# Performance work log

Measured on AMD Instinct MI355X. Metric: run time of the kernel, lower is better.

The kernel has to match this reference:

```python
import jax, jax.numpy as jnp
import numpy as np

WIN = 400   # args.win_size
K = 8       # args.topk_k


def setup_inputs() -> dict:
    key = jax.random.key(0)
    k1, k2, k3 = jax.random.split(key, 3)
    mixed = jax.random.normal(k1, (2, 400000), dtype=jnp.float32)       # [bs, n_snps]
    ref = jax.random.normal(k2, (3, 64, 400000), dtype=jnp.float32)     # [n_anc, n_refs, n_snps]
    weights = jax.random.uniform(k3, (K, 1), dtype=jnp.float32)         # AddPoolings.weights
    return {"mixed": mixed, "ref": ref, "weights": weights}


def reference(mixed, ref, weights):
    # fast_windowed_distances: broadcast multiply then windowed mean
    # mixed: [B, S], ref: [A, R, S] -> prod: [B, A, R, S]
    prod = mixed[:, None, None, :] * ref[None, :, :, :]
    B, A, R, S = prod.shape
    n_windows = S // WIN
    win_mean = prod.reshape(B, A, R, n_windows, WIN).mean(axis=-1)  # [B, A, R, W]
    # TopKPool.shared_refpanel: topk over the reference dim (R)
    scores = jnp.transpose(win_mean, (0, 1, 3, 2))       # [B, A, W, R]
    vals, idx = jax.lax.top_k(scores, K)                 # [B, A, W, K]
    # AddPoolings.shared_refpanel: weighted sum over the k dim
    out = jnp.sum(vals * weights[:K, 0], axis=-1)        # [B, A, W]
    return out, idx
```

## Files before the change

### kernel.cpp

```cpp
#include <hip/hip_runtime.h>
#include <math.h>

#define WIN   400
#define NREF  64
#define KTOP  8
#define NSNP  400000
#define NB    2
#define NA    3
#define NW    1000

__global__ __launch_bounds__(256, 4) void topk_window_kernel(
    const float* __restrict__ mixed,
    const float* __restrict__ ref,
    const float* __restrict__ weights,
    float* __restrict__ out)
{
    __shared__ float smix[NB][WIN];
    __shared__ float winvals[NB][NREF];

    const int bid  = blockIdx.x;
    const int a    = bid / NW;
    const int w    = bid % NW;
    const int tid  = threadIdx.x;
    const int lane = tid & 63;
    const int wave = tid >> 6;

    if (tid < NB * (WIN / 4)) {
        const int b  = tid / (WIN / 4);
        const int j4 = tid % (WIN / 4);
        const float4 v =
            reinterpret_cast<const float4*>(mixed + (size_t)b * NSNP + (size_t)w * WIN)[j4];
        reinterpret_cast<float4*>(&smix[b][0])[j4] = v;
    }
    __syncthreads();

    const float4* m0p = reinterpret_cast<const float4*>(&smix[0][0]);
    const float4* m1p = reinterpret_cast<const float4*>(&smix[1][0]);
    for (int r = wave; r < NREF; r += 4) {
        const float4* row = reinterpret_cast<const float4*>(
            ref + (size_t)(a * NREF + r) * NSNP + (size_t)w * WIN);
        float4 rv = row[lane];
        float4 m0 = m0p[lane];
        float4 m1 = m1p[lane];
        float acc0 = rv.x * m0.x + rv.y * m0.y + rv.z * m0.z + rv.w * m0.w;
        float acc1 = rv.x * m1.x + rv.y * m1.y + rv.z * m1.z + rv.w * m1.w;
        if (lane < (WIN / 4) - 64) {
            float4 rv2 = row[lane + 64];
            float4 n0  = m0p[lane + 64];
            float4 n1  = m1p[lane + 64];
            acc0 += rv2.x * n0.x + rv2.y * n0.y + rv2.z * n0.z + rv2.w * n0.w;
            acc1 += rv2.x * n1.x + rv2.y * n1.y + rv2.z * n1.z + rv2.w * n1.w;
        }
        #pragma unroll
        for (int off = 32; off > 0; off >>= 1) {
            acc0 += __shfl_xor(acc0, off, 64);
            acc1 += __shfl_xor(acc1, off, 64);
        }
        if (lane == 0) {
            winvals[0][r] = acc0 * (1.0f / WIN);
            winvals[1][r] = acc1 * (1.0f / WIN);
        }
    }
    __syncthreads();

    if (wave < NB) {
        const int b  = wave;
        float myval  = winvals[b][lane];
        float wsum   = 0.0f;
        float idxs[KTOP];
        #pragma unroll
        for (int k = 0; k < KTOP; ++k) {
            float v = myval;
            int   i = lane;
            #pragma unroll
            for (int off = 32; off > 0; off >>= 1) {
                float v2 = __shfl_xor(v, off, 64);
                int   i2 = __shfl_xor(i, off, 64);
                if (v2 > v || (v2 == v && i2 < i)) { v = v2; i = i2; }
            }
            wsum   += weights[k] * v;
            idxs[k] = (float)i;
            if (lane == i) myval = -INFINITY;
        }
        if (lane == 0) {
            const int ow = (b * NA + a) * NW + w;
            out[ow] = wsum;
            float4* op = reinterpret_cast<float4*>(out + (size_t)NB * NA * NW + (size_t)ow * KTOP);
            op[0] = make_float4(idxs[0], idxs[1], idxs[2], idxs[3]);
            op[1] = make_float4(idxs[4], idxs[5], idxs[6], idxs[7]);
        }
    }
}

extern "C" void kernel_launch(void* const* d_in, const int* in_sizes, int n_in,
                              void* d_out, int out_size, void* d_ws, size_t ws_size,
                              hipStream_t stream) {
    const float* mixed   = (const float*)d_in[0];
    const float* ref     = (const float*)d_in[1];
    const float* weights = (const float*)d_in[2];
    float* out = (float*)d_out;
    topk_window_kernel<<<NA * NW, 256, 0, stream>>>(mixed, ref, weights, out);
}
```

Baseline: 413.7 us.

## Split into windowed-mean and top-k kernels with per-reference contiguous tiles

Replaces the fused per-window kernel with two kernels. The first has each block process one reference row over a contiguous tile of 10 windows, staging ref and both mixed rows in shared memory and writing window means to workspace. The second does the wave-level top-k and weighted sum. The aim is longer contiguous ref reads per block instead of many 1.6KB strided segments. The cost is re-reading mixed once per reference row, a workspace round trip and an extra launch.

```diff
diff --git a/kernel.cpp b/kernel.cpp
--- a/kernel.cpp
+++ b/kernel.cpp
@@ -8,87 +8,109 @@
 #define NB    2
 #define NA    3
 #define NW    1000
+#define WT    10
+#define NWT   (NW / WT)
+#define TILE_F4 (WT * WIN / 4)
 
-__global__ __launch_bounds__(256, 4) void topk_window_kernel(
+__global__ __launch_bounds__(256) void win_mean_kernel(
     const float* __restrict__ mixed,
     const float* __restrict__ ref,
-    const float* __restrict__ weights,
-    float* __restrict__ out)
+    float* __restrict__ wmean)
 {
-    __shared__ float smix[NB][WIN];
-    __shared__ float winvals[NB][NREF];
+    __shared__ float4 sref[TILE_F4];
+    __shared__ float4 smx0[TILE_F4];
+    __shared__ float4 smx1[TILE_F4];
+    __shared__ float  part0[256];
+    __shared__ float  part1[256];
 
-    const int bid  = blockIdx.x;
-    const int a    = bid / NW;
-    const int w    = bid % NW;
-    const int tid  = threadIdx.x;
-    const int lane = tid & 63;
-    const int wave = tid >> 6;
+    const int bid = blockIdx.x;
+    const int a   = bid / (NREF * NWT);
+    const int rem = bid % (NREF * NWT);
+    const int r   = rem / NWT;
+    const int wt  = rem % NWT;
+    const int t   = threadIdx.x;
 
-    if (tid < NB * (WIN / 4)) {
-        const int b  = tid / (WIN / 4);
-        const int j4 = tid % (WIN / 4);
-        const float4 v =
-            reinterpret_cast<const float4*>(mixed + (size_t)b * NSNP + (size_t)w * WIN)[j4];
-        reinterpret_cast<float4*>(&smix[b][0])[j4] = v;
-    }
-    __syncthreads();
+    const float4* gref = reinterpret_cast<const float4*>(
+        ref + (size_t)(a * NREF + r) * NSNP + (size_t)wt * WT * WIN);
+    const float4* gm0 = reinterpret_cast<const float4*>(
+        mixed + (size_t)wt * WT * WIN);
+    const float4* gm1 = reinterpret_cast<const float4*>(
+        mixed + (size_t)NSNP + (size_t)wt * WT * WIN);
 
-    const float4* m0p = reinterpret_cast<const float4*>(&smix[0][0]);
-    const float4* m1p = reinterpret_cast<const float4*>(&smix[1][0]);
-    for (int r = wave; r < NREF; r += 4) {
-        const float4* row = reinterpret_cast<const float4*>(
-            ref + (size_t)(a * NREF + r) * NSNP + (size_t)w * WIN);
-        float4 rv = row[lane];
-        float4 m0 = m0p[lane];
-        float4 m1 = m1p[lane];
-        float acc0 = rv.x * m0.x + rv.y * m0.y + rv.z * m0.z + rv.w * m0.w;
-        float acc1 = rv.x * m1.x + rv.y * m1.y + rv.z * m1.z + rv.w * m1.w;
-        if (lane < (WIN / 4) - 64) {
-            float4 rv2 = row[lane + 64];
-            float4 n0  = m0p[lane + 64];
-            float4 n1  = m1p[lane + 64];
-            acc0 += rv2.x * n0.x + rv2.y * n0.y + rv2.z * n0.z + rv2.w * n0.w;
-            acc1 += rv2.x * n1.x + rv2.y * n1.y + rv2.z * n1.z + rv2.w * n1.w;
-        }
-        #pragma unroll
-        for (int off = 32; off > 0; off >>= 1) {
-            acc0 += __shfl_xor(acc0, off, 64);
-            acc1 += __shfl_xor(acc1, off, 64);
-        }
-        if (lane == 0) {
-            winvals[0][r] = acc0 * (1.0f / WIN);
-            winvals[1][r] = acc1 * (1.0f / WIN);
+    #pragma unroll
+    for (int j = 0; j < 4; ++j) {
+        const int idx = t + 256 * j;
+        if (idx < TILE_F4) {
+            sref[idx] = gref[idx];
+            smx0[idx] = gm0[idx];
+            smx1[idx] = gm1[idx];
         }
     }
     __syncthreads();
 
-    if (wave < NB) {
-        const int b  = wave;
-        float myval  = winvals[b][lane];
-        float wsum   = 0.0f;
-        float idxs[KTOP];
+    if (t < WT * 25) {
+        const int wloc = t / 25;
+        const int s    = t % 25;
+        float acc0 = 0.0f, acc1 = 0.0f;
         #pragma unroll
-        for (int k = 0; k < KTOP; ++k) {
-            float v = myval;
-            int   i = lane;
-            #pragma unroll
-            for (int off = 32; off > 0; off >>= 1) {
-                float v2 = __shfl_xor(v, off, 64);
-                int   i2 = __shfl_xor(i, off, 64);
-                if (v2 > v || (v2 == v && i2 < i)) { v = v2; i = i2; }
-            }
-            wsum   += weights[k] * v;
-            idxs[k] = (float)i;
-            if (lane == i) myval = -INFINITY;
+        for (int i = 0; i < 4; ++i) {
+            const int f = wloc * 100 + s + 25 * i;
+            const float4 rv = sref[f];
+            const float4 m0 = smx0[f];
+            const float4 m1 = smx1[f];
+            acc0 += rv.x * m0.x + rv.y * m0.y + rv.z * m0.z + rv.w * m0.w;
+            acc1 += rv.x * m1.x + rv.y * m1.y + rv.z * m1.z + rv.w * m1.w;
         }
-        if (lane == 0) {
-            const int ow = (b * NA + a) * NW + w;
-            out[ow] = wsum;
-            float4* op = reinterpret_cast<float4*>(out + (size_t)NB * NA * NW + (size_t)ow * KTOP);
-            op[0] = make_float4(idxs[0], idxs[1], idxs[2], idxs[3]);
-            op[1] = make_float4(idxs[4], idxs[5], idxs[6], idxs[7]);
+        part0[t] = acc0;
+        part1[t] = acc1;
+    }
+    __syncthreads();
+
+    if (t < 2 * WT) {
+        const int b    = t & 1;
+        const int wloc = t >> 1;
+        const float* p = b ? part1 : part0;
+        float s = 0.0f;
+        #pragma unroll
+        for (int i = 0; i < 25; ++i) s += p[wloc * 25 + i];
+        const int w = wt * WT + wloc;
+        wmean[(((size_t)b * NA + a) * NW + w) * NREF + r] = s * (1.0f / WIN);
+    }
+}
+
+__global__ __launch_bounds__(256) void topk_kernel(
+    const float* __restrict__ wmean,
+    const float* __restrict__ weights,
+    float* __restrict__ out)
+{
+    const int lane = threadIdx.x & 63;
+    const int wave = threadIdx.x >> 6;
+    const int g    = blockIdx.x * 4 + wave;
+    if (g >= NB * NA * NW) return;
+
+    float myval = wmean[(size_t)g * NREF + lane];
+    float wsum  = 0.0f;
+    float idxs[KTOP];
+    #pragma unroll
+    for (int k = 0; k < KTOP; ++k) {
+        float v = myval;
+        int   i = lane;
+        #pragma unroll
+        for (int off = 32; off > 0; off >>= 1) {
+            float v2 = __shfl_xor(v, off, 64);
+            int   i2 = __shfl_xor(i, off, 64);
+            if (v2 > v || (v2 == v && i2 < i)) { v = v2; i = i2; }
         }
+        wsum   += weights[k] * v;
+        idxs[k] = (float)i;
+        if (lane == i) myval = -INFINITY;
+    }
+    if (lane == 0) {
+        out[g] = wsum;
+        float4* op = reinterpret_cast<float4*>(
+            out + (size_t)NB * NA * NW + (size_t)g * KTOP);
+        op[0] = make_float4(idxs[0], idxs[1], idxs[2], idxs[3]);
+        op[1] = make_float4(idxs[4], idxs[5], idxs[6], idxs[7]);
     }
 }
 
@@ -98,6 +120,9 @@
     const float* mixed   = (const float*)d_in[0];
     const float* ref     = (const float*)d_in[1];
     const float* weights = (const float*)d_in[2];
-    float* out = (float*)d_out;
-    topk_window_kernel<<<NA * NW, 256, 0, stream>>>(mixed, ref, weights, out);
+    float* out   = (float*)d_out;
+    float* wmean = (float*)d_ws;
+
+    win_mean_kernel<<<NA * NREF * NWT, 256, 0, stream>>>(mixed, ref, wmean);
+    topk_kernel<<<(NB * NA * NW + 3) / 4, 256, 0, stream>>>(wmean, weights, out);
 }
```

After: 426.8 us. +3.2%, slower.

## Stage reference half-windows into LDS via async global_load_lds and split dot products

Applied to the files above, without the earlier changes.

The kernel now copies each half window of all 64 reference rows, plus the mixed vectors, straight into shared memory with asynchronous global-to-LDS 16-byte loads. Each wave issues sixteen row loads at once, so many more memory requests are in flight than with the earlier one-row-at-a-time loop. Each thread then computes partial dot products for one reference row over a segment of the window, and the per-wave partials are summed through shared memory, which removes the wavefront shuffle reductions. In exchange it uses about 51KB of LDS per block, lowers the launch-bounds occupancy hint, adds barriers between the load and compute phases, and the strided row reads from LDS may cause bank conflicts.

```diff
diff --git a/kernel.cpp b/kernel.cpp
--- a/kernel.cpp
+++ b/kernel.cpp
@@ -8,65 +8,80 @@
 #define NB    2
 #define NA    3
 #define NW    1000
+#define HF4   50
 
-__global__ __launch_bounds__(256, 4) void topk_window_kernel(
+__device__ __forceinline__ void async_copy16(void* lds, const void* g) {
+    __builtin_amdgcn_global_load_lds(
+        (const __attribute__((address_space(1))) unsigned int*)g,
+        (__attribute__((address_space(3))) unsigned int*)lds,
+        16, 0, 0);
+}
+
+__global__ __launch_bounds__(256, 2) void fused_kernel(
     const float* __restrict__ mixed,
     const float* __restrict__ ref,
     const float* __restrict__ weights,
     float* __restrict__ out)
 {
-    __shared__ float smix[NB][WIN];
-    __shared__ float winvals[NB][NREF];
+    __shared__ float4 sref[NREF * HF4];
+    __shared__ float4 smix[2 * 100];
+    __shared__ float  part[NB][4][NREF];
 
     const int bid  = blockIdx.x;
     const int a    = bid / NW;
     const int w    = bid % NW;
-    const int tid  = threadIdx.x;
-    const int lane = tid & 63;
-    const int wave = tid >> 6;
+    const int t    = threadIdx.x;
+    const int lane = t & 63;
+    const int wv   = t >> 6;
 
-    if (tid < NB * (WIN / 4)) {
-        const int b  = tid / (WIN / 4);
-        const int j4 = tid % (WIN / 4);
-        const float4 v =
-            reinterpret_cast<const float4*>(mixed + (size_t)b * NSNP + (size_t)w * WIN)[j4];
-        reinterpret_cast<float4*>(&smix[b][0])[j4] = v;
+    const int r   = lane;
+    const int seg = wv;
+    const int st  = seg * 13 - (seg == 3 ? 1 : 0);
+    const int len = (seg < 2) ? 13 : 12;
+
+    float acc0 = 0.0f, acc1 = 0.0f;
+
+    for (int h = 0; h < 2; ++h) {
+        const float* gbase = ref + (size_t)(a * NREF + wv * 16) * NSNP
+                                 + (size_t)w * WIN + h * (WIN / 2);
+        #pragma unroll
+        for (int j = 0; j < 16; ++j) {
+            const float4* g =
+                reinterpret_cast<const float4*>(gbase + (size_t)j * NSNP) + lane;
+            if (lane < HF4)
+                async_copy16(&sref[(wv * 16 + j) * HF4], g);
+        }
+        if (h == 0 && wv < NB) {
+            const float4* gm = reinterpret_cast<const float4*>(
+                mixed + (size_t)wv * NSNP + (size_t)w * WIN);
+            async_copy16(&smix[wv * 100], gm + lane);
+            if (lane < 36)
+                async_copy16(&smix[wv * 100 + 64], gm + 64 + lane);
+        }
+        __syncthreads();
+
+        const float4* rp = &sref[r * HF4 + st];
+        const float4* m0 = &smix[0 * 100 + h * HF4 + st];
+        const float4* m1 = &smix[1 * 100 + h * HF4 + st];
+        for (int i = 0; i < len; ++i) {
+            const float4 rv = rp[i];
+            const float4 x0 = m0[i];
+            const float4 x1 = m1[i];
+            acc0 += rv.x * x0.x + rv.y * x0.y + rv.z * x0.z + rv.w * x0.w;
+            acc1 += rv.x * x1.x + rv.y * x1.y + rv.z * x1.z + rv.w * x1.w;
+        }
+        __syncthreads();
     }
+
+    part[0][seg][r] = acc0;
+    part[1][seg][r] = acc1;
     __syncthreads();
 
-    const float4* m0p = reinterpret_cast<const float4*>(&smix[0][0]);
-    const float4* m1p = reinterpret_cast<const float4*>(&smix[1][0]);
-    for (int r = wave; r < NREF; r += 4) {
-        const float4* row = reinterpret_cast<const float4*>(
-            ref + (size_t)(a * NREF + r) * NSNP + (size_t)w * WIN);
-        float4 rv = row[lane];
-        float4 m0 = m0p[lane];
-        float4 m1 = m1p[lane];
-        float acc0 = rv.x * m0.x + rv.y * m0.y + rv.z * m0.z + rv.w * m0.w;
-        float acc1 = rv.x * m1.x + rv.y * m1.y + rv.z * m1.z + rv.w * m1.w;
-        if (lane < (WIN / 4) - 64) {
-            float4 rv2 = row[lane + 64];
-            float4 n0  = m0p[lane + 64];
-            float4 n1  = m1p[lane + 64];
-            acc0 += rv2.x * n0.x + rv2.y * n0.y + rv2.z * n0.z + rv2.w * n0.w;
-            acc1 += rv2.x * n1.x + rv2.y * n1.y + rv2.z * n1.z + rv2.w * n1.w;
-        }
-        #pragma unroll
-        for (int off = 32; off > 0; off >>= 1) {
-            acc0 += __shfl_xor(acc0, off, 64);
-            acc1 += __shfl_xor(acc1, off, 64);
-        }
-        if (lane == 0) {
-            winvals[0][r] = acc0 * (1.0f / WIN);
-            winvals[1][r] = acc1 * (1.0f / WIN);
-        }
-    }
-    __syncthreads();
-
-    if (wave < NB) {
-        const int b  = wave;
-        float myval  = winvals[b][lane];
-        float wsum   = 0.0f;
+    if (wv < NB) {
+        const int b = wv;
+        float myval = (part[b][0][lane] + part[b][1][lane] +
+                       part[b][2][lane] + part[b][3][lane]) * (1.0f / WIN);
+        float wsum  = 0.0f;
         float idxs[KTOP];
         #pragma unroll
         for (int k = 0; k < KTOP; ++k) {
@@ -83,9 +98,10 @@
             if (lane == i) myval = -INFINITY;
         }
         if (lane == 0) {
-            const int ow = (b * NA + a) * NW + w;
-            out[ow] = wsum;
-            float4* op = reinterpret_cast<float4*>(out + (size_t)NB * NA * NW + (size_t)ow * KTOP);
+            const int g = (b * NA + a) * NW + w;
+            out[g] = wsum;
+            float4* op = reinterpret_cast<float4*>(
+                out + (size_t)NB * NA * NW + (size_t)g * KTOP);
             op[0] = make_float4(idxs[0], idxs[1], idxs[2], idxs[3]);
             op[1] = make_float4(idxs[4], idxs[5], idxs[6], idxs[7]);
         }
@@ -99,5 +115,5 @@
     const float* ref     = (const float*)d_in[1];
     const float* weights = (const float*)d_in[2];
     float* out = (float*)d_out;
-    topk_window_kernel<<<NA * NW, 256, 0, stream>>>(mixed, ref, weights, out);
+    fused_kernel<<<NA * NW, 256, 0, stream>>>(mixed, ref, weights, out);
 }
```

Result: no change. 414.4 us (+0.2%).
